# Kernel tuning notes

Measured on AMD Instinct MI355X. Metric: run time of the kernel, lower is better.

The kernel has to match this reference:

```python
import jax, jax.numpy as jnp
import numpy as np

B, N, M, C, H, G, KD = 4, 1024, 128, 512, 8, 3, 16
DH = C // H


def setup_inputs() -> dict:
    key = jax.random.key(0)
    ks = jax.random.split(key, 12)
    def w(k, shape, fan_in):
        return jax.random.normal(k, shape, jnp.float32) / np.sqrt(fan_in)
    return {
        'pairwise_g': jax.random.normal(ks[0], (B, N, N, G), jnp.float32),
        'coset_functions': jax.random.normal(ks[1], (B, N, C), jnp.float32),
        'mask': jnp.ones((B, N), dtype=bool),
        'W1': w(ks[2], (G, KD), G), 'b1': jnp.zeros((KD,), jnp.float32),
        'W2': w(ks[3], (KD, KD), KD), 'b2': jnp.zeros((KD,), jnp.float32),
        'W3': w(ks[4], (KD, H), KD), 'b3': jnp.zeros((H,), jnp.float32),
        'Wq': w(ks[5], (C, C), C), 'bq': jnp.zeros((C,), jnp.float32),
        'Wk': w(ks[6], (C, C), C), 'bk': jnp.zeros((C,), jnp.float32),
        'Wv': w(ks[7], (C, C), C), 'bv': jnp.zeros((C,), jnp.float32),
        'Wo': w(ks[8], (C, C), C), 'bo': jnp.zeros((C,), jnp.float32),
    }


def _gather_nbhd(x, idx):
    # x: (B, N, ...) gathered along point axis with idx: (B, Nq, M) -> (B, Nq, M, ...)
    return jax.vmap(lambda a, i: a[i])(x, idx)


def reference(pairwise_g, coset_functions, mask,
              W1, b1, W2, b2, W3, b3,
              Wq, bq, Wk, bk, Wv, bv, Wo, bo):
    swish = jax.nn.silu
    # --- neighborhood extraction: topk smallest group distance (mc_samples path) ---
    dists = jnp.linalg.norm(pairwise_g, axis=-1)                  # (B,N,N)
    dists = jnp.where(mask[:, None, :], dists, jnp.float32(1e8))
    _, nbhd_idx = jax.lax.top_k(-dists, M)                        # (B,N,M) nearest M

    nbhd_g = jnp.take_along_axis(pairwise_g, nbhd_idx[..., None], axis=2)  # (B,N,M,G)
    nbhd_mask = _gather_nbhd(mask, nbhd_idx)                      # (B,N,M)

    # --- location kernel: per-pair MLP on lie-algebra offsets -> per-head logits ---
    h = swish(nbhd_g @ W1 + b1)
    h = swish(h @ W2 + b2)
    loc = h @ W3 + b3                                             # (B,N,M,H)

    # --- feature kernel: multi-head dot product, keys gathered at neighborhoods ---
    q = (coset_functions @ Wq + bq).reshape(B, N, H, DH)
    k = coset_functions @ Wk + bk                                 # (B,N,C)
    k_n = _gather_nbhd(k, nbhd_idx).reshape(B, N, M, H, DH)
    dot = jnp.einsum('bnhd,bnmhd->bnmh', q, k_n) / jnp.sqrt(jnp.float32(DH))

    # --- masked softmax over neighborhood axis ---
    pre = loc + dot
    pre = jnp.where(nbhd_mask[..., None], pre, jnp.float32(-1e38))
    attn = jax.nn.softmax(pre, axis=2)                            # (B,N,M,H)

    # --- value projection, gather, weighted aggregate, output projection ---
    v = coset_functions @ Wv + bv                                 # (B,N,C)
    v_n = _gather_nbhd(v, nbhd_idx).reshape(B, N, M, H, DH)
    out = jnp.einsum('bnmh,bnmhd->bnhd', attn, v_n).reshape(B, N, C)
    out = out @ Wo + bo                                           # (B,N,C)
    return out
```

## Files before the change

kernel.cpp:

```cpp
#include <hip/hip_runtime.h>
#include <hip/hip_bf16.h>
#include <math.h>

#define NB 4
#define NPTS 1024
#define MN 128
#define CH 512
#define NH 8
#define DHD 64
#define NG 3
#define KDIM 16

typedef unsigned short u16;
typedef unsigned short u16x8 __attribute__((ext_vector_type(8)));
typedef short short8 __attribute__((ext_vector_type(8)));
typedef float f32x4 __attribute__((ext_vector_type(4)));

__device__ __forceinline__ float b2f(u16 u) {
  return __uint_as_float(((unsigned)u) << 16);
}
__device__ __forceinline__ u16 f2b(float f) {
  unsigned x = __float_as_uint(f);
  return (u16)((x + 0x7FFFu + ((x >> 16) & 1u)) >> 16);
}

__global__ __launch_bounds__(256) void cvt_bf16(const float* __restrict__ x,
                                                u16* __restrict__ y) {
  int i = blockIdx.x * 256 + threadIdx.x;
  float4 a = ((const float4*)x)[i * 2];
  float4 b = ((const float4*)x)[i * 2 + 1];
  ushort4 o0, o1;
  o0.x = f2b(a.x); o0.y = f2b(a.y); o0.z = f2b(a.z); o0.w = f2b(a.w);
  o1.x = f2b(b.x); o1.y = f2b(b.y); o1.z = f2b(b.z); o1.w = f2b(b.w);
  ((ushort4*)y)[i * 2] = o0;
  ((ushort4*)y)[i * 2 + 1] = o1;
}

__global__ __launch_bounds__(256) void transpose_cvt(
    const float* __restrict__ W0, const float* __restrict__ W1,
    const float* __restrict__ W2, const float* __restrict__ W3,
    u16* __restrict__ T0, u16* __restrict__ T1, u16* __restrict__ T2,
    u16* __restrict__ T3) {
  const float* src; u16* dst;
  if (blockIdx.z == 0)      { src = W0; dst = T0; }
  else if (blockIdx.z == 1) { src = W1; dst = T1; }
  else if (blockIdx.z == 2) { src = W2; dst = T2; }
  else                      { src = W3; dst = T3; }
  __shared__ float tile[32][33];
  const int k0 = blockIdx.y * 32, n0 = blockIdx.x * 32;
  const int r8 = threadIdx.x >> 5, c = threadIdx.x & 31;
#pragma unroll
  for (int i = 0; i < 4; i++)
    tile[r8 + i * 8][c] = src[(size_t)(k0 + r8 + i * 8) * CH + n0 + c];
  __syncthreads();
#pragma unroll
  for (int i = 0; i < 4; i++)
    dst[(size_t)(n0 + r8 + i * 8) * CH + k0 + c] = f2b(tile[c][r8 + i * 8]);
}

__device__ __forceinline__ void gstore(float* p, float v) { *p = v; }
__device__ __forceinline__ void gstore(u16* p, float v) { *p = f2b(v); }

template <typename OT>
__global__ __launch_bounds__(256) void mfma_gemm3(
    const u16* __restrict__ A,
    const u16* __restrict__ Wa, const float* __restrict__ ba,
    const u16* __restrict__ Wb, const float* __restrict__ bb_,
    const u16* __restrict__ Wc, const float* __restrict__ bc,
    OT* __restrict__ Ya, OT* __restrict__ Yb, OT* __restrict__ Yc) {
  const u16* W; const float* bias; OT* Y;
  if (blockIdx.z == 0)      { W = Wa; bias = ba;  Y = Ya; }
  else if (blockIdx.z == 1) { W = Wb; bias = bb_; Y = Yb; }
  else                      { W = Wc; bias = bc;  Y = Yc; }

  __shared__ u16 As[128][40];
  __shared__ u16 Bs[128][40];

  const int t = threadIdx.x;
  const int row0 = blockIdx.y * 128;
  const int col0 = blockIdx.x * 128;
  const int r2 = t >> 1;
  const int sb = (t & 1) * 16;
  const int w = t >> 6, lane = t & 63;
  const int q4 = lane >> 4, l16 = lane & 15;
  const int wr = (w & 1) * 64, wc = (w >> 1) * 64;

  f32x4 acc[4][4];
#pragma unroll
  for (int mt = 0; mt < 4; mt++)
#pragma unroll
    for (int nt = 0; nt < 4; nt++) acc[mt][nt] = (f32x4){0.f, 0.f, 0.f, 0.f};

  for (int kt = 0; kt < CH; kt += 32) {
    u16x8 av0 = *(const u16x8*)(A + (size_t)(row0 + r2) * CH + kt + sb);
    u16x8 av1 = *(const u16x8*)(A + (size_t)(row0 + r2) * CH + kt + sb + 8);
    u16x8 bv0 = *(const u16x8*)(W + (size_t)(col0 + r2) * CH + kt + sb);
    u16x8 bv1 = *(const u16x8*)(W + (size_t)(col0 + r2) * CH + kt + sb + 8);
    *(u16x8*)&As[r2][sb] = av0;
    *(u16x8*)&As[r2][sb + 8] = av1;
    *(u16x8*)&Bs[r2][sb] = bv0;
    *(u16x8*)&Bs[r2][sb + 8] = bv1;
    __syncthreads();
    short8 af[4], bf[4];
#pragma unroll
    for (int mt = 0; mt < 4; mt++)
      af[mt] = *(const short8*)&As[wr + mt * 16 + l16][q4 * 8];
#pragma unroll
    for (int nt = 0; nt < 4; nt++)
      bf[nt] = *(const short8*)&Bs[wc + nt * 16 + l16][q4 * 8];
#pragma unroll
    for (int mt = 0; mt < 4; mt++)
#pragma unroll
      for (int nt = 0; nt < 4; nt++)
        acc[mt][nt] = __builtin_amdgcn_mfma_f32_16x16x32_bf16(
            af[mt], bf[nt], acc[mt][nt], 0, 0, 0);
    __syncthreads();
  }

#pragma unroll
  for (int nt = 0; nt < 4; nt++) {
    const int col = col0 + wc + nt * 16 + l16;
    const float bb = bias[col];
#pragma unroll
    for (int mt = 0; mt < 4; mt++) {
#pragma unroll
      for (int r = 0; r < 4; r++) {
        const int row = row0 + wr + mt * 16 + q4 * 4 + r;
        gstore(Y + (size_t)row * CH + col, acc[mt][nt][r] + bb);
      }
    }
  }
}

__global__ __launch_bounds__(256) void select_topk(const float* __restrict__ g,
                                                   int* __restrict__ idx_out) {
  const int bn = blockIdx.x;
  const int t = threadIdx.x;
  __shared__ unsigned int key[NPTS];
  __shared__ int hist[256];
  __shared__ int incl[256];
  __shared__ unsigned int s_prefix;
  __shared__ int s_target;
  __shared__ int s_cless;
  __shared__ int s_ctie;
  __shared__ int s_fill;

  const float* row = g + (size_t)bn * (NPTS * NG);
#pragma unroll
  for (int r = 0; r < 4; r++) {
    int j = t + 256 * r;
    float g0 = row[j * 3 + 0];
    float g1 = row[j * 3 + 1];
    float g2 = row[j * 3 + 2];
    float ss = __fadd_rn(__fadd_rn(__fmul_rn(g0, g0), __fmul_rn(g1, g1)),
                         __fmul_rn(g2, g2));
    float d = __fsqrt_rn(ss);
    key[j] = __float_as_uint(d);
  }
  if (t == 0) { s_prefix = 0u; s_target = MN - 1; }
  __syncthreads();

  for (int pass = 3; pass >= 0; pass--) {
    const unsigned int pref = s_prefix;
    const int target = s_target;
    const int sh = 8 * pass;
    const unsigned int himask = (pass == 3) ? 0u : (0xFFFFFFFFu << (sh + 8));
    hist[t] = 0;
    __syncthreads();
#pragma unroll
    for (int r = 0; r < 4; r++) {
      unsigned int kk = key[t + 256 * r];
      if ((kk & himask) == (pref & himask))
        atomicAdd(&hist[(kk >> sh) & 255], 1);
    }
    __syncthreads();
    incl[t] = hist[t];
    __syncthreads();
    for (int off = 1; off < 256; off <<= 1) {
      int add = (t >= off) ? incl[t - off] : 0;
      __syncthreads();
      incl[t] += add;
      __syncthreads();
    }
    int below = (t == 0) ? 0 : incl[t - 1];
    int mine = incl[t];
    __syncthreads();
    if (mine > target && below <= target) {
      s_prefix = pref | ((unsigned int)t << sh);
      s_target = target - below;
    }
    __syncthreads();
  }

  const unsigned int T = s_prefix;
  const int need = s_target + 1;
  if (t == 0) { s_cless = 0; s_ctie = 0; s_fill = 0; }
  __syncthreads();
  int* orow = idx_out + bn * MN;
#pragma unroll
  for (int r = 0; r < 4; r++) {
    int j = t + 256 * r;
    unsigned int kk = key[j];
    if (kk < T) {
      int p = atomicAdd(&s_cless, 1);
      if (p < MN) orow[p] = j;
    } else if (kk == T) {
      atomicAdd(&s_ctie, 1);
    }
  }
  __syncthreads();
  const int L = s_cless;
  const int ctie = s_ctie;
  __syncthreads();
  if (ctie == need) {
    for (int r = 0; r < 4; r++) {
      int j = t + 256 * r;
      if (key[j] == T) {
        int p = atomicAdd(&s_fill, 1);
        int q = L + p;
        if (q < MN) orow[q] = j;
      }
    }
  } else {
    for (int r = 0; r < 4; r++) {
      int j = t + 256 * r;
      if (key[j] == T) {
        int rank = 0;
        for (int jj = 0; jj < j; jj++) rank += (key[jj] == T) ? 1 : 0;
        int q = L + rank;
        if (rank < need && q >= 0 && q < MN) orow[q] = j;
      }
    }
  }
}

__global__ __launch_bounds__(128) void loc_mlp(
    const float* __restrict__ pgin, const int* __restrict__ idxg,
    const float* __restrict__ W1, const float* __restrict__ b1,
    const float* __restrict__ W2, const float* __restrict__ b2,
    const float* __restrict__ W3, const float* __restrict__ b3,
    u16* __restrict__ locw) {
  const int bn = blockIdx.x;
  const int t = threadIdx.x;
  const int j = idxg[bn * MN + t] & (NPTS - 1);
  const float* gp = pgin + ((size_t)bn * NPTS + j) * NG;
  float g0 = gp[0], g1 = gp[1], g2 = gp[2];
  float h1[KDIM], h2[KDIM];
#pragma unroll
  for (int u = 0; u < KDIM; u++) {
    float s = W1[u] * g0 + W1[KDIM + u] * g1 + W1[2 * KDIM + u] * g2 + b1[u];
    h1[u] = s / (1.f + expf(-s));
  }
#pragma unroll
  for (int vv = 0; vv < KDIM; vv++) {
    float s = b2[vv];
#pragma unroll
    for (int u = 0; u < KDIM; u++) s += h1[u] * W2[u * KDIM + vv];
    h2[vv] = s / (1.f + expf(-s));
  }
  u16* op = locw + ((size_t)bn * MN + t) * NH;
#pragma unroll
  for (int h = 0; h < NH; h++) {
    float s = b3[h];
#pragma unroll
    for (int vv = 0; vv < KDIM; vv++) s += h2[vv] * W3[vv * NH + h];
    op[h] = f2b(s);
  }
}

#define WPB 4

__global__ __launch_bounds__(256) void attn_kernel(
    const u16* __restrict__ qg, const u16* __restrict__ kg,
    const u16* __restrict__ vg, const u16* __restrict__ locw,
    const int* __restrict__ idxg, u16* __restrict__ outg) {
  const int t = threadIdx.x;
  const int wv = t >> 6;
  const int lane = t & 63;
  const int bn = blockIdx.x * WPB + wv;
  const int b = bn >> 10;

  __shared__ int nidx[WPB][MN];
  nidx[wv][lane] = idxg[bn * MN + lane] & (NPTS - 1);
  nidx[wv][lane + 64] = idxg[bn * MN + 64 + lane] & (NPTS - 1);
  __syncthreads();

  u16x8 qv = *(const u16x8*)(qg + (size_t)bn * CH + lane * 8);
  float q[8];
#pragma unroll
  for (int e = 0; e < 8; e++) q[e] = b2f(qv[e]);
  const int hl = lane >> 3;
  const u16* kb = kg + (size_t)b * NPTS * CH;
  const u16* vb = vg + (size_t)b * NPTS * CH;
  const u16* lb = locw + (size_t)bn * MN * NH;

  float M = -INFINITY, L = 0.f;
  float a[8];
#pragma unroll
  for (int e = 0; e < 8; e++) a[e] = 0.f;

  for (int m = 0; m < MN; m += 2) {
    const int j0 = nidx[wv][m];
    const int j1 = nidx[wv][m + 1];
    u16x8 k0v = *(const u16x8*)(kb + (size_t)j0 * CH + lane * 8);
    u16x8 k1v = *(const u16x8*)(kb + (size_t)j1 * CH + lane * 8);
    u16x8 v0v = *(const u16x8*)(vb + (size_t)j0 * CH + lane * 8);
    u16x8 v1v = *(const u16x8*)(vb + (size_t)j1 * CH + lane * 8);
    float l0 = b2f(lb[m * NH + hl]);
    float l1 = b2f(lb[(m + 1) * NH + hl]);

    float p0 = 0.f, p1 = 0.f;
#pragma unroll
    for (int e = 0; e < 8; e++) {
      p0 += q[e] * b2f(k0v[e]);
      p1 += q[e] * b2f(k1v[e]);
    }
    p0 += __shfl_xor(p0, 1); p0 += __shfl_xor(p0, 2); p0 += __shfl_xor(p0, 4);
    p1 += __shfl_xor(p1, 1); p1 += __shfl_xor(p1, 2); p1 += __shfl_xor(p1, 4);
    p0 = p0 * 0.125f + l0;
    p1 = p1 * 0.125f + l1;

    float mx = fmaxf(M, fmaxf(p0, p1));
    float alpha = expf(M - mx);
    float e0 = expf(p0 - mx);
    float e1 = expf(p1 - mx);
    L = L * alpha + e0 + e1;
#pragma unroll
    for (int e = 0; e < 8; e++)
      a[e] = a[e] * alpha + e0 * b2f(v0v[e]) + e1 * b2f(v1v[e]);
    M = mx;
  }

  const float inv = 1.f / L;
  u16x8 o;
#pragma unroll
  for (int e = 0; e < 8; e++) o[e] = f2b(a[e] * inv);
  *(u16x8*)(outg + (size_t)bn * CH + lane * 8) = o;
}

extern "C" void kernel_launch(void* const* d_in, const int* in_sizes, int n_in,
                              void* d_out, int out_size, void* d_ws, size_t ws_size,
                              hipStream_t stream) {
  (void)in_sizes; (void)n_in; (void)out_size; (void)ws_size;
  const float* pg = (const float*)d_in[0];
  const float* cf = (const float*)d_in[1];
  const float* W1 = (const float*)d_in[3];
  const float* b1 = (const float*)d_in[4];
  const float* W2 = (const float*)d_in[5];
  const float* b2 = (const float*)d_in[6];
  const float* W3 = (const float*)d_in[7];
  const float* b3 = (const float*)d_in[8];
  const float* Wq = (const float*)d_in[9];
  const float* bq = (const float*)d_in[10];
  const float* Wk = (const float*)d_in[11];
  const float* bk = (const float*)d_in[12];
  const float* Wv = (const float*)d_in[13];
  const float* bv = (const float*)d_in[14];
  const float* Wo = (const float*)d_in[15];
  const float* bo = (const float*)d_in[16];
  float* out = (float*)d_out;

  char* p = (char*)d_ws;
  u16* cfb = (u16*)p;
  u16* WTq = (u16*)(p + (4 << 20));
  u16* WTk = WTq + 262144;
  u16* WTv = WTk + 262144;
  u16* WTo = WTv + 262144;
  u16* qw = (u16*)(p + (6 << 20));
  u16* kw = (u16*)(p + (10 << 20));
  u16* vw = (u16*)(p + (14 << 20));
  int* idxw = (int*)(p + (18 << 20));
  u16* locw = (u16*)(p + (20 << 20));
  u16* awb = qw;

  const int R = NB * NPTS;

  cvt_bf16<<<dim3(R * CH / 8 / 256), 256, 0, stream>>>(cf, cfb);
  transpose_cvt<<<dim3(16, 16, 4), 256, 0, stream>>>(Wq, Wk, Wv, Wo, WTq, WTk,
                                                     WTv, WTo);
  mfma_gemm3<u16><<<dim3(CH / 128, R / 128, 3), 256, 0, stream>>>(
      cfb, WTq, bq, WTk, bk, WTv, bv, qw, kw, vw);
  select_topk<<<dim3(R), 256, 0, stream>>>(pg, idxw);
  loc_mlp<<<dim3(R), 128, 0, stream>>>(pg, idxw, W1, b1, W2, b2, W3, b3, locw);
  attn_kernel<<<dim3(R / WPB), 256, 0, stream>>>(qw, kw, vw, locw, idxw, awb);
  mfma_gemm3<float><<<dim3(CH / 128, R / 128, 1), 256, 0, stream>>>(
      awb, WTo, bo, WTo, bo, WTo, bo, out, out, out);
}
```

Measured before the change: 266.8 us.

## Fuse top-k selection with location MLP and speed up radix select

```diff
diff --git a/kernel.cpp b/kernel.cpp
--- a/kernel.cpp
+++ b/kernel.cpp
@@ -15,6 +15,8 @@
 typedef unsigned short u16x8 __attribute__((ext_vector_type(8)));
 typedef short short8 __attribute__((ext_vector_type(8)));
 typedef float f32x4 __attribute__((ext_vector_type(4)));
+
+#define FEXP(x) __expf(x)
 
 __device__ __forceinline__ float b2f(u16 u) {
   return __uint_as_float(((unsigned)u) << 16);
@@ -132,18 +134,23 @@
   }
 }
 
-__global__ __launch_bounds__(256) void select_topk(const float* __restrict__ g,
-                                                   int* __restrict__ idx_out) {
+__global__ __launch_bounds__(256) void select_loc(
+    const float* __restrict__ g, int* __restrict__ idx_out,
+    const float* __restrict__ W1, const float* __restrict__ b1,
+    const float* __restrict__ W2, const float* __restrict__ b2,
+    const float* __restrict__ W3, const float* __restrict__ b3,
+    u16* __restrict__ locw) {
   const int bn = blockIdx.x;
   const int t = threadIdx.x;
+  const int wv = t >> 6, lane = t & 63;
   __shared__ unsigned int key[NPTS];
-  __shared__ int hist[256];
+  __shared__ int hist[4][256];
   __shared__ int incl[256];
+  __shared__ int wtot[4];
+  __shared__ int selidx[MN];
   __shared__ unsigned int s_prefix;
-  __shared__ int s_target;
-  __shared__ int s_cless;
-  __shared__ int s_ctie;
-  __shared__ int s_fill;
+  __shared__ unsigned int s_selmask;
+  __shared__ int s_target, s_done, s_cless, s_ctie, s_fill;
 
   const float* row = g + (size_t)bn * (NPTS * NG);
 #pragma unroll
@@ -154,44 +161,59 @@
     float g2 = row[j * 3 + 2];
     float ss = __fadd_rn(__fadd_rn(__fmul_rn(g0, g0), __fmul_rn(g1, g1)),
                          __fmul_rn(g2, g2));
-    float d = __fsqrt_rn(ss);
-    key[j] = __float_as_uint(d);
-  }
-  if (t == 0) { s_prefix = 0u; s_target = MN - 1; }
+    key[j] = __float_as_uint(__fsqrt_rn(ss));
+  }
+  if (t == 0) {
+    s_prefix = 0u; s_target = MN - 1; s_done = 0;
+    s_selmask = 0xFFFFFFFFu;
+  }
   __syncthreads();
 
   for (int pass = 3; pass >= 0; pass--) {
+    if (s_done) break;
     const unsigned int pref = s_prefix;
     const int target = s_target;
     const int sh = 8 * pass;
     const unsigned int himask = (pass == 3) ? 0u : (0xFFFFFFFFu << (sh + 8));
-    hist[t] = 0;
+#pragma unroll
+    for (int w = 0; w < 4; w++) hist[w][t] = 0;
     __syncthreads();
 #pragma unroll
     for (int r = 0; r < 4; r++) {
       unsigned int kk = key[t + 256 * r];
       if ((kk & himask) == (pref & himask))
-        atomicAdd(&hist[(kk >> sh) & 255], 1);
-    }
-    __syncthreads();
-    incl[t] = hist[t];
-    __syncthreads();
-    for (int off = 1; off < 256; off <<= 1) {
-      int add = (t >= off) ? incl[t - off] : 0;
-      __syncthreads();
-      incl[t] += add;
-      __syncthreads();
-    }
+        atomicAdd(&hist[wv][(kk >> sh) & 255], 1);
+    }
+    __syncthreads();
+    int sv = hist[0][t] + hist[1][t] + hist[2][t] + hist[3][t];
+#pragma unroll
+    for (int o = 1; o < 64; o <<= 1) {
+      int n = __shfl_up(sv, o);
+      if (lane >= o) sv += n;
+    }
+    if (lane == 63) wtot[wv] = sv;
+    __syncthreads();
+    int base = 0;
+#pragma unroll
+    for (int w = 0; w < 4; w++) base += (w < wv) ? wtot[w] : 0;
+    sv += base;
+    incl[t] = sv;
+    __syncthreads();
     int below = (t == 0) ? 0 : incl[t - 1];
     int mine = incl[t];
     __syncthreads();
     if (mine > target && below <= target) {
       s_prefix = pref | ((unsigned int)t << sh);
       s_target = target - below;
-    }
-    __syncthreads();
-  }
-
+      if (mine - below == target - below + 1) {
+        s_done = 1;
+        s_selmask = 0xFFFFFFFFu << sh;
+      }
+    }
+    __syncthreads();
+  }
+
+  const unsigned int sm = s_selmask;
   const unsigned int T = s_prefix;
   const int need = s_target + 1;
   if (t == 0) { s_cless = 0; s_ctie = 0; s_fill = 0; }
@@ -200,10 +222,10 @@
 #pragma unroll
   for (int r = 0; r < 4; r++) {
     int j = t + 256 * r;
-    unsigned int kk = key[j];
+    unsigned int kk = key[j] & sm;
     if (kk < T) {
       int p = atomicAdd(&s_cless, 1);
-      if (p < MN) orow[p] = j;
+      if (p < MN) { orow[p] = j; selidx[p] = j; }
     } else if (kk == T) {
       atomicAdd(&s_ctie, 1);
     }
@@ -215,56 +237,50 @@
   if (ctie == need) {
     for (int r = 0; r < 4; r++) {
       int j = t + 256 * r;
-      if (key[j] == T) {
+      if ((key[j] & sm) == T) {
         int p = atomicAdd(&s_fill, 1);
         int q = L + p;
-        if (q < MN) orow[q] = j;
+        if (q < MN) { orow[q] = j; selidx[q] = j; }
       }
     }
   } else {
     for (int r = 0; r < 4; r++) {
       int j = t + 256 * r;
-      if (key[j] == T) {
+      if ((key[j] & sm) == T) {
         int rank = 0;
-        for (int jj = 0; jj < j; jj++) rank += (key[jj] == T) ? 1 : 0;
+        for (int jj = 0; jj < j; jj++) rank += ((key[jj] & sm) == T) ? 1 : 0;
         int q = L + rank;
-        if (rank < need && q >= 0 && q < MN) orow[q] = j;
+        if (rank < need && q >= 0 && q < MN) { orow[q] = j; selidx[q] = j; }
       }
     }
   }
-}
-
-__global__ __launch_bounds__(128) void loc_mlp(
-    const float* __restrict__ pgin, const int* __restrict__ idxg,
-    const float* __restrict__ W1, const float* __restrict__ b1,
-    const float* __restrict__ W2, const float* __restrict__ b2,
-    const float* __restrict__ W3, const float* __restrict__ b3,
-    u16* __restrict__ locw) {
-  const int bn = blockIdx.x;
-  const int t = threadIdx.x;
-  const int j = idxg[bn * MN + t] & (NPTS - 1);
-  const float* gp = pgin + ((size_t)bn * NPTS + j) * NG;
-  float g0 = gp[0], g1 = gp[1], g2 = gp[2];
-  float h1[KDIM], h2[KDIM];
-#pragma unroll
-  for (int u = 0; u < KDIM; u++) {
-    float s = W1[u] * g0 + W1[KDIM + u] * g1 + W1[2 * KDIM + u] * g2 + b1[u];
-    h1[u] = s / (1.f + expf(-s));
-  }
-#pragma unroll
-  for (int vv = 0; vv < KDIM; vv++) {
-    float s = b2[vv];
-#pragma unroll
-    for (int u = 0; u < KDIM; u++) s += h1[u] * W2[u * KDIM + vv];
-    h2[vv] = s / (1.f + expf(-s));
-  }
-  u16* op = locw + ((size_t)bn * MN + t) * NH;
-#pragma unroll
-  for (int h = 0; h < NH; h++) {
-    float s = b3[h];
-#pragma unroll
-    for (int vv = 0; vv < KDIM; vv++) s += h2[vv] * W3[vv * NH + h];
-    op[h] = f2b(s);
+  __syncthreads();
+
+  if (t < MN) {
+    const int j = selidx[t] & (NPTS - 1);
+    const float* gp = g + ((size_t)bn * NPTS + j) * NG;
+    float g0 = gp[0], g1 = gp[1], g2 = gp[2];
+    float h1[KDIM], h2[KDIM];
+#pragma unroll
+    for (int u = 0; u < KDIM; u++) {
+      float s = W1[u] * g0 + W1[KDIM + u] * g1 + W1[2 * KDIM + u] * g2 + b1[u];
+      h1[u] = s / (1.f + FEXP(-s));
+    }
+#pragma unroll
+    for (int vv = 0; vv < KDIM; vv++) {
+      float s = b2[vv];
+#pragma unroll
+      for (int u = 0; u < KDIM; u++) s += h1[u] * W2[u * KDIM + vv];
+      h2[vv] = s / (1.f + FEXP(-s));
+    }
+    u16* op = locw + ((size_t)bn * MN + t) * NH;
+#pragma unroll
+    for (int h = 0; h < NH; h++) {
+      float s = b3[h];
+#pragma unroll
+      for (int vv = 0; vv < KDIM; vv++) s += h2[vv] * W3[vv * NH + h];
+      op[h] = f2b(s);
+    }
   }
 }
 
@@ -321,9 +337,9 @@
     p1 = p1 * 0.125f + l1;
 
     float mx = fmaxf(M, fmaxf(p0, p1));
-    float alpha = expf(M - mx);
-    float e0 = expf(p0 - mx);
-    float e1 = expf(p1 - mx);
+    float alpha = FEXP(M - mx);
+    float e0 = FEXP(p0 - mx);
+    float e1 = FEXP(p1 - mx);
     L = L * alpha + e0 + e1;
 #pragma unroll
     for (int e = 0; e < 8; e++)
@@ -380,8 +396,8 @@
                                                      WTv, WTo);
   mfma_gemm3<u16><<<dim3(CH / 128, R / 128, 3), 256, 0, stream>>>(
       cfb, WTq, bq, WTk, bk, WTv, bv, qw, kw, vw);
-  select_topk<<<dim3(R), 256, 0, stream>>>(pg, idxw);
-  loc_mlp<<<dim3(R), 128, 0, stream>>>(pg, idxw, W1, b1, W2, b2, W3, b3, locw);
+  select_loc<<<dim3(R), 256, 0, stream>>>(pg, idxw, W1, b1, W2, b2, W3, b3,
+                                          locw);
   attn_kernel<<<dim3(R / WPB), 256, 0, stream>>>(qw, kw, vw, locw, idxw, awb);
   mfma_gemm3<float><<<dim3(CH / 128, R / 128, 1), 256, 0, stream>>>(
       awb, WTo, bo, WTo, bo, WTo, bo, out, out, out);
```

Result: faster. 246.8 us (-7.5%).
